# Kernel tuning notes

Hardware: AMD Instinct MI355X
Metric: run time of the kernel (lower is better)

The kernel has to match this reference:

```python
import jax, jax.numpy as jnp
import numpy as np


def setup_inputs() -> dict:
    key = jax.random.key(0)
    k1, k2, k3 = jax.random.split(key, 3)
    B, H, D, N = 2, 16, 64, 2048
    return {
        "query": jax.random.normal(k1, (B, H, D, N), dtype=jnp.float32),
        "key": jax.random.normal(k2, (B, H, D, N), dtype=jnp.float32),
        "value": jax.random.normal(k3, (B, H, D, N), dtype=jnp.float32),
    }


def reference(query, key, value):
    # NOTE: original torch code scales by sqrt(query.size(-1)) which,
    # given the [B,H,d,N] layout, is sqrt(N) (the sequence length), not sqrt(d).
    scale = query.shape[-1] ** 0.5
    # scores[b,h,q,k] = sum_d query[b,h,d,q] * key[b,h,d,k]
    scores = jnp.einsum("bhdq,bhdk->bhqk", query, key) / scale
    attn = jax.nn.softmax(scores, axis=-1)
    # out[b,h,q,v] = sum_k attn[b,h,q,k] * value[b,h,v,k]
    return jnp.einsum("bhqk,bhvk->bhqv", attn, value)
```

## Files before the change

kernel.cpp:

```cpp
#include <hip/hip_runtime.h>
#include <hip/hip_bf16.h>


typedef __attribute__((ext_vector_type(8))) short short8;
typedef __attribute__((ext_vector_type(4))) float f32x4;

#define NN 2048
#define DD 64
#define ROWB 144

#if __has_builtin(__builtin_amdgcn_exp2f)
#define EXP2(x) __builtin_amdgcn_exp2f(x)
#else
#define EXP2(x) __expf(0.69314718056f * (x))
#endif

__device__ __forceinline__ unsigned pk2(float a, float b) {
  __hip_bfloat162 h = __float22bfloat162_rn(make_float2(a, b));
  unsigned u; __builtin_memcpy(&u, &h, 4); return u;
}
__device__ __forceinline__ short f2bf(float f) {
  union { float f; unsigned u; } x; x.f = f;
  unsigned r = (x.u + 0x7fffu + ((x.u >> 16) & 1u)) >> 16;
  return (short)r;
}

__global__ __launch_bounds__(256, 2) void attn_kernel(
    const float* __restrict__ Q, const float* __restrict__ K,
    const float* __restrict__ V, float* __restrict__ Out) {
  const int tid  = threadIdx.x;
  const int wave = tid >> 6, lane = tid & 63;
  const int quad = lane >> 4, l16 = lane & 15;

  const int bh   = blockIdx.x >> 4;
  const int qblk = blockIdx.x & 15;

  const float* Qh = Q + (size_t)bh * DD * NN;
  const float* Kh = K + (size_t)bh * DD * NN;
  const float* Vh = V + (size_t)bh * DD * NN;
  float*       Oh = Out + (size_t)bh * NN * DD;

  __shared__ __align__(16) char ldsK[64 * ROWB];
  __shared__ __align__(16) char ldsV[64 * ROWB];
  __shared__ __align__(16) char ldsP[8][16 * ROWB];

  const float qscale = 0.031881407f;
  short8 bQ[2][2];
  int qb[2];
#pragma unroll
  for (int qt = 0; qt < 2; ++qt) {
    qb[qt] = qblk * 128 + (wave * 2 + qt) * 16;
#pragma unroll
    for (int h = 0; h < 2; ++h)
#pragma unroll
      for (int j = 0; j < 8; ++j) {
        int d = h * 32 + quad * 8 + j;
        bQ[qt][h][j] = f2bf(Qh[(size_t)d * NN + qb[qt] + l16] * qscale);
      }
  }

  f32x4 accO[2][4];
#pragma unroll
  for (int qt = 0; qt < 2; ++qt)
#pragma unroll
    for (int vt = 0; vt < 4; ++vt) accO[qt][vt] = (f32x4){0.f, 0.f, 0.f, 0.f};
  float lp[2] = {0.f, 0.f};

  const int ka = tid & 31, kg = tid >> 5;
  const int vv = tid >> 2, vko = (tid & 3) * 16;
  char* Pq0 = ldsP[wave * 2];
  char* Pq1 = ldsP[wave * 2 + 1];
  const int swr = l16 >> 1;

  for (int k0 = 0; k0 < NN; k0 += 64) {
    __syncthreads();
    {
      const float* kp0 = Kh + (size_t)(2 * ka) * NN + k0 + kg * 8;
      const float* kp1 = kp0 + NN;
      float4 a0 = ((const float4*)kp0)[0], a1 = ((const float4*)kp0)[1];
      float4 b0 = ((const float4*)kp1)[0], b1 = ((const float4*)kp1)[1];
      float r0[8] = {a0.x, a0.y, a0.z, a0.w, a1.x, a1.y, a1.z, a1.w};
      float r1[8] = {b0.x, b0.y, b0.z, b0.w, b1.x, b1.y, b1.z, b1.w};
#pragma unroll
      for (int j = 0; j < 8; ++j) {
        int k = kg * 8 + j;
        int grp = (ka >> 2) ^ ((k >> 1) & 7);
        *(unsigned*)&ldsK[k * ROWB + grp * 16 + (ka & 3) * 4] = pk2(r0[j], r1[j]);
      }
      const float* vp = Vh + (size_t)vv * NN + k0 + vko;
      float4 c0 = ((const float4*)vp)[0], c1 = ((const float4*)vp)[1];
      float4 c2 = ((const float4*)vp)[2], c3 = ((const float4*)vp)[3];
      uint4 w0 = make_uint4(pk2(c0.x, c0.y), pk2(c0.z, c0.w), pk2(c1.x, c1.y), pk2(c1.z, c1.w));
      uint4 w1 = make_uint4(pk2(c2.x, c2.y), pk2(c2.z, c2.w), pk2(c3.x, c3.y), pk2(c3.z, c3.w));
      *(uint4*)&ldsV[vv * ROWB + vko * 2]      = w0;
      *(uint4*)&ldsV[vv * ROWB + vko * 2 + 16] = w1;
    }
    __syncthreads();

    f32x4 s[2][4];
#pragma unroll
    for (int kt = 0; kt < 4; ++kt) {
      const int key = kt * 16 + l16;
      short8 aK0 = *(const short8*)&ldsK[key * ROWB + ((quad) ^ swr) * 16];
      short8 aK1 = *(const short8*)&ldsK[key * ROWB + ((4 + quad) ^ swr) * 16];
      f32x4 z = (f32x4){0.f, 0.f, 0.f, 0.f};
      s[0][kt] = __builtin_amdgcn_mfma_f32_16x16x32_bf16(aK0, bQ[0][0], z, 0, 0, 0);
      s[0][kt] = __builtin_amdgcn_mfma_f32_16x16x32_bf16(aK1, bQ[0][1], s[0][kt], 0, 0, 0);
      s[1][kt] = __builtin_amdgcn_mfma_f32_16x16x32_bf16(aK0, bQ[1][0], z, 0, 0, 0);
      s[1][kt] = __builtin_amdgcn_mfma_f32_16x16x32_bf16(aK1, bQ[1][1], s[1][kt], 0, 0, 0);
    }

#pragma unroll
    for (int qt = 0; qt < 2; ++qt) {
      char* Pq = qt ? Pq1 : Pq0;
#pragma unroll
      for (int kt = 0; kt < 4; ++kt) {
        float p0 = EXP2(s[qt][kt][0]);
        float p1 = EXP2(s[qt][kt][1]);
        float p2 = EXP2(s[qt][kt][2]);
        float p3 = EXP2(s[qt][kt][3]);
        lp[qt] += (p0 + p1) + (p2 + p3);
        uint2 w; w.x = pk2(p0, p1); w.y = pk2(p2, p3);
        *(uint2*)&Pq[l16 * ROWB + kt * 32 + quad * 8] = w;
      }
    }

#pragma unroll
    for (int h2 = 0; h2 < 2; ++h2) {
      short8 aP0 = *(const short8*)&Pq0[l16 * ROWB + h2 * 64 + quad * 16];
      short8 aP1 = *(const short8*)&Pq1[l16 * ROWB + h2 * 64 + quad * 16];
#pragma unroll
      for (int vt = 0; vt < 4; ++vt) {
        short8 bV = *(const short8*)&ldsV[(vt * 16 + l16) * ROWB + h2 * 64 + quad * 16];
        accO[0][vt] = __builtin_amdgcn_mfma_f32_16x16x32_bf16(aP0, bV, accO[0][vt], 0, 0, 0);
        accO[1][vt] = __builtin_amdgcn_mfma_f32_16x16x32_bf16(aP1, bV, accO[1][vt], 0, 0, 0);
      }
    }
  }

#pragma unroll
  for (int qt = 0; qt < 2; ++qt) {
    float l = lp[qt];
    l += __shfl_xor(l, 16, 64);
    l += __shfl_xor(l, 32, 64);
#pragma unroll
    for (int r = 0; r < 4; ++r) {
      float lr  = __shfl(l, quad * 4 + r, 64);
      float inv = 1.0f / lr;
      int q = qb[qt] + quad * 4 + r;
#pragma unroll
      for (int vt = 0; vt < 4; ++vt)
        Oh[(size_t)q * DD + vt * 16 + l16] = accO[qt][vt][r] * inv;
    }
  }
}

extern "C" void kernel_launch(void* const* d_in, const int* in_sizes, int n_in,
                              void* d_out, int out_size, void* d_ws, size_t ws_size,
                              hipStream_t stream) {
  const float* Q = (const float*)d_in[0];
  const float* K = (const float*)d_in[1];
  const float* V = (const float*)d_in[2];
  float* O = (float*)d_out;
  dim3 grid(2 * 16 * (NN / 128));
  attn_kernel<<<grid, dim3(256), 0, stream>>>(Q, K, V, O);
}
```

Measured before the change: 165.2 us.

## Double-buffer K/V tiles in LDS and prefetch next tile into registers

Adds a second LDS buffer for K and V. The global loads for the next 64-key tile are issued before the current tile's MFMA work, and the converted tile is stored into the alternate buffer afterward. This cuts one barrier per iteration and hides global load latency behind compute. The cost is more LDS (two extra ~9KB buffers, which may lower occupancy) and 32 extra live registers for the prefetched floats. The last iteration does a redundant wrap-around load of tile 0.

Measured after the change: 138.1 us. -16.4%, faster.

```diff
diff --git a/kernel.cpp b/kernel.cpp
--- a/kernel.cpp
+++ b/kernel.cpp
@@ -40,8 +40,8 @@
   const float* Vh = V + (size_t)bh * DD * NN;
   float*       Oh = Out + (size_t)bh * NN * DD;
 
-  __shared__ __align__(16) char ldsK[64 * ROWB];
-  __shared__ __align__(16) char ldsV[64 * ROWB];
+  __shared__ __align__(16) char ldsK[2][64 * ROWB];
+  __shared__ __align__(16) char ldsV[2][64 * ROWB];
   __shared__ __align__(16) char ldsP[8][16 * ROWB];
 
   const float qscale = 0.031881407f;
@@ -68,41 +68,62 @@
 
   const int ka = tid & 31, kg = tid >> 5;
   const int vv = tid >> 2, vko = (tid & 3) * 16;
+  const float* kbase0 = Kh + (size_t)(2 * ka) * NN + kg * 8;
+  const float* kbase1 = kbase0 + NN;
+  const float* vbase  = Vh + (size_t)vv * NN + vko;
   char* Pq0 = ldsP[wave * 2];
   char* Pq1 = ldsP[wave * 2 + 1];
   const int swr = l16 >> 1;
 
-  for (int k0 = 0; k0 < NN; k0 += 64) {
-    __syncthreads();
-    {
-      const float* kp0 = Kh + (size_t)(2 * ka) * NN + k0 + kg * 8;
-      const float* kp1 = kp0 + NN;
-      float4 a0 = ((const float4*)kp0)[0], a1 = ((const float4*)kp0)[1];
-      float4 b0 = ((const float4*)kp1)[0], b1 = ((const float4*)kp1)[1];
-      float r0[8] = {a0.x, a0.y, a0.z, a0.w, a1.x, a1.y, a1.z, a1.w};
-      float r1[8] = {b0.x, b0.y, b0.z, b0.w, b1.x, b1.y, b1.z, b1.w};
+  float kA[8], kB[8], vA[16];
+  auto load_kv = [&](int k0) {
+    const float4* p0 = (const float4*)(kbase0 + k0);
+    const float4* p1 = (const float4*)(kbase1 + k0);
+    float4 a0 = p0[0], a1 = p0[1];
+    float4 b0 = p1[0], b1 = p1[1];
+    kA[0] = a0.x; kA[1] = a0.y; kA[2] = a0.z; kA[3] = a0.w;
+    kA[4] = a1.x; kA[5] = a1.y; kA[6] = a1.z; kA[7] = a1.w;
+    kB[0] = b0.x; kB[1] = b0.y; kB[2] = b0.z; kB[3] = b0.w;
+    kB[4] = b1.x; kB[5] = b1.y; kB[6] = b1.z; kB[7] = b1.w;
+    const float4* pv = (const float4*)(vbase + k0);
+    float4 c0 = pv[0], c1 = pv[1], c2 = pv[2], c3 = pv[3];
+    vA[0]  = c0.x; vA[1]  = c0.y; vA[2]  = c0.z; vA[3]  = c0.w;
+    vA[4]  = c1.x; vA[5]  = c1.y; vA[6]  = c1.z; vA[7]  = c1.w;
+    vA[8]  = c2.x; vA[9]  = c2.y; vA[10] = c2.z; vA[11] = c2.w;
+    vA[12] = c3.x; vA[13] = c3.y; vA[14] = c3.z; vA[15] = c3.w;
+  };
+  auto store_kv = [&](char* bK, char* bV) {
 #pragma unroll
-      for (int j = 0; j < 8; ++j) {
-        int k = kg * 8 + j;
-        int grp = (ka >> 2) ^ ((k >> 1) & 7);
-        *(unsigned*)&ldsK[k * ROWB + grp * 16 + (ka & 3) * 4] = pk2(r0[j], r1[j]);
-      }
-      const float* vp = Vh + (size_t)vv * NN + k0 + vko;
-      float4 c0 = ((const float4*)vp)[0], c1 = ((const float4*)vp)[1];
-      float4 c2 = ((const float4*)vp)[2], c3 = ((const float4*)vp)[3];
-      uint4 w0 = make_uint4(pk2(c0.x, c0.y), pk2(c0.z, c0.w), pk2(c1.x, c1.y), pk2(c1.z, c1.w));
-      uint4 w1 = make_uint4(pk2(c2.x, c2.y), pk2(c2.z, c2.w), pk2(c3.x, c3.y), pk2(c3.z, c3.w));
-      *(uint4*)&ldsV[vv * ROWB + vko * 2]      = w0;
-      *(uint4*)&ldsV[vv * ROWB + vko * 2 + 16] = w1;
+    for (int j = 0; j < 8; ++j) {
+      int k = kg * 8 + j;
+      int grp = (ka >> 2) ^ ((k >> 1) & 7);
+      *(unsigned*)&bK[k * ROWB + grp * 16 + (ka & 3) * 4] = pk2(kA[j], kB[j]);
     }
-    __syncthreads();
+    uint4 w0 = make_uint4(pk2(vA[0], vA[1]),  pk2(vA[2], vA[3]),
+                          pk2(vA[4], vA[5]),  pk2(vA[6], vA[7]));
+    uint4 w1 = make_uint4(pk2(vA[8], vA[9]),  pk2(vA[10], vA[11]),
+                          pk2(vA[12], vA[13]), pk2(vA[14], vA[15]));
+    *(uint4*)&bV[vv * ROWB + vko * 2]      = w0;
+    *(uint4*)&bV[vv * ROWB + vko * 2 + 16] = w1;
+  };
+
+  load_kv(0);
+  store_kv(ldsK[0], ldsV[0]);
+  __syncthreads();
+
+  for (int it = 0; it < 32; ++it) {
+    const int cur = it & 1;
+    load_kv(((it + 1) & 31) * 64);
+
+    const char* cK = ldsK[cur];
+    const char* cV = ldsV[cur];
 
     f32x4 s[2][4];
 #pragma unroll
     for (int kt = 0; kt < 4; ++kt) {
       const int key = kt * 16 + l16;
-      short8 aK0 = *(const short8*)&ldsK[key * ROWB + ((quad) ^ swr) * 16];
-      short8 aK1 = *(const short8*)&ldsK[key * ROWB + ((4 + quad) ^ swr) * 16];
+      short8 aK0 = *(const short8*)&cK[key * ROWB + ((quad) ^ swr) * 16];
+      short8 aK1 = *(const short8*)&cK[key * ROWB + ((4 + quad) ^ swr) * 16];
       f32x4 z = (f32x4){0.f, 0.f, 0.f, 0.f};
       s[0][kt] = __builtin_amdgcn_mfma_f32_16x16x32_bf16(aK0, bQ[0][0], z, 0, 0, 0);
       s[0][kt] = __builtin_amdgcn_mfma_f32_16x16x32_bf16(aK1, bQ[0][1], s[0][kt], 0, 0, 0);
@@ -131,11 +152,14 @@
       short8 aP1 = *(const short8*)&Pq1[l16 * ROWB + h2 * 64 + quad * 16];
 #pragma unroll
       for (int vt = 0; vt < 4; ++vt) {
-        short8 bV = *(const short8*)&ldsV[(vt * 16 + l16) * ROWB + h2 * 64 + quad * 16];
+        short8 bV = *(const short8*)&cV[(vt * 16 + l16) * ROWB + h2 * 64 + quad * 16];
         accO[0][vt] = __builtin_amdgcn_mfma_f32_16x16x32_bf16(aP0, bV, accO[0][vt], 0, 0, 0);
         accO[1][vt] = __builtin_amdgcn_mfma_f32_16x16x32_bf16(aP1, bV, accO[1][vt], 0, 0, 0);
       }
     }
+
+    store_kv(ldsK[cur ^ 1], ldsV[cur ^ 1]);
+    __syncthreads();
   }
 
 #pragma unroll
```
